# Performance work log

Hardware: AMD Instinct MI355X
Metric: run time of the kernel (lower is better)

## Reference

```python
import jax, jax.numpy as jnp
import numpy as np

DIM = 512
EPS = 1e-08
LN_EPS = 1e-05  # torch LayerNorm default


def layer_norm(x, g, b):
    mu = jnp.mean(x, axis=-1, keepdims=True)
    var = jnp.mean(jnp.square(x - mu), axis=-1, keepdims=True)
    return (x - mu) * jax.lax.rsqrt(var + LN_EPS) * g + b


def setup_inputs() -> dict:
    key = jax.random.key(0)
    ks = jax.random.split(key, 10)
    B, NQ, NK, D = 8, 1024, 2048, DIM
    s = 1.0 / np.sqrt(D)
    return {
        "inputs": jax.random.normal(ks[0], (B, NQ, D), jnp.float32),
        "context": jax.random.normal(ks[1], (B, NK, D), jnp.float32),
        "ln_in_g": jnp.ones((D,), jnp.float32),
        "ln_in_b": jnp.zeros((D,), jnp.float32),
        "ln_ctx_g": jnp.ones((D,), jnp.float32),
        "ln_ctx_b": jnp.zeros((D,), jnp.float32),
        "Wq": jax.random.uniform(ks[2], (D, D), jnp.float32, -s, s),
        "bq": jax.random.uniform(ks[3], (D,), jnp.float32, -s, s),
        "Wk": jax.random.uniform(ks[4], (D, D), jnp.float32, -s, s),
        "bk": jax.random.uniform(ks[5], (D,), jnp.float32, -s, s),
        "Wv": jax.random.uniform(ks[6], (D, D), jnp.float32, -s, s),
        "bv": jax.random.uniform(ks[7], (D,), jnp.float32, -s, s),
    }


def reference(inputs, context, ln_in_g, ln_in_b, ln_ctx_g, ln_ctx_b, Wq, bq, Wk, bk, Wv, bv):
    x = layer_norm(inputs, ln_in_g, ln_in_b)
    c = layer_norm(context, ln_ctx_g, ln_ctx_b)
    q = x @ Wq.T + bq  # [B, Nq, D]
    k = c @ Wk.T + bk  # [B, Nk, D]
    v = c @ Wv.T + bv  # [B, Nk, D]
    scale = DIM ** (-0.5)
    dots = jnp.einsum('bid,bjd->bij', q, k) * scale  # [B, Nq, Nk]
    attn = jax.nn.softmax(dots, axis=1) + EPS  # softmax over query axis
    attn = attn / jnp.sum(attn, axis=2, keepdims=True)  # renorm over key axis
    updates = jnp.einsum('bjd,bij->bid', v, attn)
    return updates
```

## Files before the change

kernel.cpp:

```cpp
#include <hip/hip_runtime.h>

using u16 = unsigned short;
typedef __attribute__((ext_vector_type(8))) short short8;
typedef __attribute__((ext_vector_type(4))) float floatx4;

#define NQ 1024
#define NK 2048
#define DD 512

__device__ __forceinline__ float bf2f(u16 u) {
  union { unsigned u; float f; } x; x.u = ((unsigned)u) << 16; return x.f;
}
__device__ __forceinline__ unsigned cvt_pk_bf16(float lo, float hi) {
  unsigned r;
  asm("v_cvt_pk_bf16_f32 %0, %1, %2" : "=v"(r) : "v"(lo), "v"(hi));
  return r;
}
__device__ __forceinline__ float wave_sum(float v) {
#pragma unroll
  for (int off = 32; off > 0; off >>= 1) v += __shfl_down(v, off, 64);
  return v;
}
__device__ __forceinline__ void gload16(const u16* g, const u16* l) {
  __builtin_amdgcn_global_load_lds(
      (const __attribute__((address_space(1))) void*)g,
      (__attribute__((address_space(3))) void*)l, 16, 0, 0);
}

__global__ __launch_bounds__(256) void ln_prep(
    const float* __restrict__ X1, const float* __restrict__ G1,
    const float* __restrict__ B1, u16* __restrict__ Y1,
    const float* __restrict__ X2, const float* __restrict__ G2,
    const float* __restrict__ B2, u16* __restrict__ Y2,
    const float* __restrict__ Wq, const float* __restrict__ Wk,
    const float* __restrict__ Wv, u16* __restrict__ wqb,
    u16* __restrict__ wkb, u16* __restrict__ wvb, float* __restrict__ Zero,
    float qsc) {
  const int bx = blockIdx.x;
  const int t = threadIdx.x;
  if (bx >= 6144) {
    int e = bx - 6144;
    if (e < 768) {
      const float* src = e < 256 ? Wq : (e < 512 ? Wk : Wv);
      u16* dst = e < 256 ? wqb : (e < 512 ? wkb : wvb);
      const float ws = e < 256 ? qsc : 1.f;
      int i = ((e & 255) * 256 + t) * 4;
      float4 v = *(const float4*)(src + i);
      union { unsigned u[2]; ushort4 s; } ou;
      ou.u[0] = cvt_pk_bf16(v.x * ws, v.y * ws);
      ou.u[1] = cvt_pk_bf16(v.z * ws, v.w * ws);
      *(ushort4*)(dst + i) = ou.s;
    } else {
      int i = ((e - 768) * 256 + t) * 4;
      float4 z = {0.f, 0.f, 0.f, 0.f};
      *(float4*)(Zero + i) = z;
    }
    return;
  }
  const int wave = t >> 6, lane = t & 63;
  int row = bx * 4 + wave;
  const float *X, *G, *Bv; u16* Y;
  if (row < 8192) { X = X1; G = G1; Bv = B1; Y = Y1; }
  else { row -= 8192; X = X2; G = G2; Bv = B2; Y = Y2; }
  const float4* Xp = (const float4*)(X + (long)row * DD);
  float4 v0 = Xp[lane * 2], v1 = Xp[lane * 2 + 1];
  float s = v0.x + v0.y + v0.z + v0.w + v1.x + v1.y + v1.z + v1.w;
  float ss = v0.x * v0.x + v0.y * v0.y + v0.z * v0.z + v0.w * v0.w +
             v1.x * v1.x + v1.y * v1.y + v1.z * v1.z + v1.w * v1.w;
  s = wave_sum(s);  s = __shfl(s, 0, 64);
  ss = wave_sum(ss); ss = __shfl(ss, 0, 64);
  float mu = s * (1.f / DD);
  float var = ss * (1.f / DD) - mu * mu;
  float rs = rsqrtf(var + 1e-5f);
  const float4* Gp = (const float4*)G;
  const float4* Bp = (const float4*)Bv;
  float4 g0 = Gp[lane * 2], g1 = Gp[lane * 2 + 1];
  float4 b0 = Bp[lane * 2], b1 = Bp[lane * 2 + 1];
  union { unsigned u[4]; short8 s8; } ou;
  ou.u[0] = cvt_pk_bf16((v0.x - mu) * rs * g0.x + b0.x,
                        (v0.y - mu) * rs * g0.y + b0.y);
  ou.u[1] = cvt_pk_bf16((v0.z - mu) * rs * g0.z + b0.z,
                        (v0.w - mu) * rs * g0.w + b0.w);
  ou.u[2] = cvt_pk_bf16((v1.x - mu) * rs * g1.x + b1.x,
                        (v1.y - mu) * rs * g1.y + b1.y);
  ou.u[3] = cvt_pk_bf16((v1.z - mu) * rs * g1.z + b1.z,
                        (v1.w - mu) * rs * g1.w + b1.w);
  *(short8*)(Y + (long)row * DD + lane * 8) = ou.s8;
}

__global__ __launch_bounds__(256) void gemm_proj(
    const u16* __restrict__ A1, const u16* __restrict__ W1,
    const float* __restrict__ b1, u16* __restrict__ C1,
    const u16* __restrict__ A2, const u16* __restrict__ W2,
    const float* __restrict__ b2, u16* __restrict__ C2,
    float bsc1, float bsc2) {
  __shared__ u16 smem[16384];
  u16* lA = smem;
  u16* lB = smem + 8192;
  const u16 *A, *B; const float* bias; u16* Cout; float bsc;
  int m0 = blockIdx.x * 128;
  if (blockIdx.x < 64) { A = A1; B = W1; bias = b1; Cout = C1; bsc = bsc1; }
  else { A = A2; B = W2; bias = b2; Cout = C2; bsc = bsc2;
         m0 = (blockIdx.x - 64) * 128; }
  const int n0 = blockIdx.y * 128;
  const int t = threadIdx.x, wave = t >> 6, lane = t & 63;
  const int fm = lane & 15, fq = lane >> 4;
  const int wm = (wave >> 1) * 64, wn = (wave & 1) * 64;

  const int srow = t >> 3;
  const int swz = ((t & 7) ^ (srow & 7)) * 8;
  const u16* gA = A + (long)(m0 + srow) * 512 + swz;
  const u16* gB = B + (long)(n0 + srow) * 512 + swz;
  u16* dA = lA + wave * 512;
  u16* dB = lB + wave * 512;

  floatx4 acc[4][4];
#pragma unroll
  for (int x = 0; x < 4; ++x)
#pragma unroll
    for (int y = 0; y < 4; ++y) { floatx4 z = {0.f, 0.f, 0.f, 0.f}; acc[x][y] = z; }

#pragma unroll 1
  for (int kt = 0; kt < 8; ++kt) {
    gload16(gA, dA);
    gload16(gA + 32L * 512, dA + 2048);
    gload16(gA + 64L * 512, dA + 4096);
    gload16(gA + 96L * 512, dA + 6144);
    gload16(gB, dB);
    gload16(gB + 32L * 512, dB + 2048);
    gload16(gB + 64L * 512, dB + 4096);
    gload16(gB + 96L * 512, dB + 6144);
    gA += 64; gB += 64;
    __syncthreads();
#pragma unroll
    for (int ks = 0; ks < 2; ++ks) {
      short8 af[4], bfr[4];
      const int csl = ((ks * 4 + fq) ^ (fm & 7)) * 8;
#pragma unroll
      for (int x = 0; x < 4; ++x)
        af[x] = *(const short8*)&lA[(wm + x * 16 + fm) * 64 + csl];
#pragma unroll
      for (int y = 0; y < 4; ++y)
        bfr[y] = *(const short8*)&lB[(wn + y * 16 + fm) * 64 + csl];
#pragma unroll
      for (int x = 0; x < 4; ++x)
#pragma unroll
        for (int y = 0; y < 4; ++y)
          acc[x][y] = __builtin_amdgcn_mfma_f32_16x16x32_bf16(af[x], bfr[y], acc[x][y], 0, 0, 0);
    }
    __syncthreads();
  }

  float bs[4];
  int cs[4];
#pragma unroll
  for (int y = 0; y < 4; ++y) {
    bs[y] = bias[n0 + wn + y * 16 + fm] * bsc;
    cs[y] = ((((wn >> 4) + y) ^ fq) * 16) + fm;
  }
#pragma unroll
  for (int x = 0; x < 4; ++x)
#pragma unroll
    for (int r = 0; r < 4; ++r) {
      int rowl = wm + x * 16 + fq * 4 + r;
      unsigned p01 = cvt_pk_bf16(acc[x][0][r] + bs[0], acc[x][1][r] + bs[1]);
      unsigned p23 = cvt_pk_bf16(acc[x][2][r] + bs[2], acc[x][3][r] + bs[3]);
      smem[rowl * 128 + cs[0]] = (u16)p01;
      smem[rowl * 128 + cs[1]] = (u16)(p01 >> 16);
      smem[rowl * 128 + cs[2]] = (u16)p23;
      smem[rowl * 128 + cs[3]] = (u16)(p23 >> 16);
    }
  __syncthreads();
#pragma unroll
  for (int p = 0; p < 8; ++p) {
    int rowl = p * 16 + (t >> 4);
    int c = t & 15;
    int q = (rowl >> 2) & 3;
    short8 v = *(const short8*)&smem[rowl * 128 + (((c >> 1) ^ q) * 16) + (c & 1) * 8];
    *(short8*)(Cout + (long)(m0 + rowl) * 512 + n0 + c * 8) = v;
  }
}

__global__ __launch_bounds__(256) void qk_vproj(
    const u16* __restrict__ qb, const u16* __restrict__ kb,
    u16* __restrict__ E, float* __restrict__ Z,
    const u16* __restrict__ wvb, const u16* __restrict__ cb,
    const float* __restrict__ bv, u16* __restrict__ vT,
    float* __restrict__ colV) {
  __shared__ u16 smem[16384];
  u16* lA = smem;
  u16* lB = smem + 8192;

  const int bx = blockIdx.x;
  const bool is_qk = bx < 1024;
  const u16 *A, *B;
  int m0, n0, b;
  if (is_qk) {
    b = bx & 7;
    n0 = ((bx >> 3) & 15) * 128;
    m0 = (bx >> 7) * 128;
    A = qb + (long)b * (1024L * 512);
    B = kb + (long)b * (2048L * 512);
  } else {
    int e = bx - 1024;
    m0 = (e & 3) * 128;
    n0 = (e >> 2) * 128;
    b = 0;
    A = wvb;
    B = cb;
  }
  const int t = threadIdx.x, wave = t >> 6, lane = t & 63;
  const int fm = lane & 15, fq = lane >> 4;
  const int wm = (wave >> 1) * 64, wn = (wave & 1) * 64;

  const int srow = t >> 3;
  const int swz = ((t & 7) ^ (srow & 7)) * 8;
  const u16* gA = A + (long)(m0 + srow) * 512 + swz;
  const u16* gB = B + (long)(n0 + srow) * 512 + swz;
  u16* dA = lA + wave * 512;
  u16* dB = lB + wave * 512;

  floatx4 acc[4][4];
#pragma unroll
  for (int x = 0; x < 4; ++x)
#pragma unroll
    for (int y = 0; y < 4; ++y) { floatx4 z = {0.f, 0.f, 0.f, 0.f}; acc[x][y] = z; }

#pragma unroll 1
  for (int kt = 0; kt < 8; ++kt) {
    gload16(gA, dA);
    gload16(gA + 32L * 512, dA + 2048);
    gload16(gA + 64L * 512, dA + 4096);
    gload16(gA + 96L * 512, dA + 6144);
    gload16(gB, dB);
    gload16(gB + 32L * 512, dB + 2048);
    gload16(gB + 64L * 512, dB + 4096);
    gload16(gB + 96L * 512, dB + 6144);
    gA += 64; gB += 64;
    __syncthreads();
#pragma unroll
    for (int ks = 0; ks < 2; ++ks) {
      short8 af[4], bfr[4];
      const int csl = ((ks * 4 + fq) ^ (fm & 7)) * 8;
#pragma unroll
      for (int x = 0; x < 4; ++x)
        af[x] = *(const short8*)&lA[(wm + x * 16 + fm) * 64 + csl];
#pragma unroll
      for (int y = 0; y < 4; ++y)
        bfr[y] = *(const short8*)&lB[(wn + y * 16 + fm) * 64 + csl];
#pragma unroll
      for (int x = 0; x < 4; ++x)
#pragma unroll
        for (int y = 0; y < 4; ++y)
          acc[x][y] = __builtin_amdgcn_mfma_f32_16x16x32_bf16(af[x], bfr[y], acc[x][y], 0, 0, 0);
    }
    __syncthreads();
  }

  int cs[4];
#pragma unroll
  for (int y = 0; y < 4; ++y) cs[y] = ((((wn >> 4) + y) ^ fq) * 16) + fm;

  if (is_qk) {
    float s4[4] = {0.f, 0.f, 0.f, 0.f};
#pragma unroll
    for (int x = 0; x < 4; ++x)
#pragma unroll
      for (int r = 0; r < 4; ++r) {
        int rowl = wm + x * 16 + fq * 4 + r;
        float e0 = __builtin_amdgcn_exp2f(acc[x][0][r]);
        float e1 = __builtin_amdgcn_exp2f(acc[x][1][r]);
        float e2 = __builtin_amdgcn_exp2f(acc[x][2][r]);
        float e3 = __builtin_amdgcn_exp2f(acc[x][3][r]);
        s4[0] += e0; s4[1] += e1; s4[2] += e2; s4[3] += e3;
        unsigned p01 = cvt_pk_bf16(e0, e1);
        unsigned p23 = cvt_pk_bf16(e2, e3);
        smem[rowl * 128 + cs[0]] = (u16)p01;
        smem[rowl * 128 + cs[1]] = (u16)(p01 >> 16);
        smem[rowl * 128 + cs[2]] = (u16)p23;
        smem[rowl * 128 + cs[3]] = (u16)(p23 >> 16);
      }
#pragma unroll
    for (int y = 0; y < 4; ++y) {
      s4[y] += __shfl_xor(s4[y], 16, 64);
      s4[y] += __shfl_xor(s4[y], 32, 64);
    }
    __syncthreads();
    u16* Eg = E + (long)b * (1024L * 2048);
#pragma unroll
    for (int p = 0; p < 8; ++p) {
      int rowl = p * 16 + (t >> 4);
      int c = t & 15;
      int q = (rowl >> 2) & 3;
      short8 v = *(const short8*)&smem[rowl * 128 + (((c >> 1) ^ q) * 16) + (c & 1) * 8];
      *(short8*)(Eg + (long)(m0 + rowl) * 2048 + n0 + c * 8) = v;
    }
    if (fq == 0) {
#pragma unroll
      for (int y = 0; y < 4; ++y)
        atomicAdd(&Z[b * 2048 + n0 + wn + y * 16 + fm], s4[y]);
    }
  } else {
    const int bb = n0 >> 11;
    const int j0c = n0 & 2047;
    float bsr[4][4];
#pragma unroll
    for (int x = 0; x < 4; ++x)
#pragma unroll
      for (int r = 0; r < 4; ++r)
        bsr[x][r] = bv[m0 + wm + x * 16 + fq * 4 + r];
    float rs[4][4];
#pragma unroll
    for (int x = 0; x < 4; ++x)
#pragma unroll
      for (int r = 0; r < 4; ++r) rs[x][r] = 0.f;
#pragma unroll
    for (int x = 0; x < 4; ++x)
#pragma unroll
      for (int r = 0; r < 4; ++r) {
        int rowl = wm + x * 16 + fq * 4 + r;
        float v0 = acc[x][0][r] + bsr[x][r];
        float v1 = acc[x][1][r] + bsr[x][r];
        float v2 = acc[x][2][r] + bsr[x][r];
        float v3 = acc[x][3][r] + bsr[x][r];
        rs[x][r] += v0 + v1 + v2 + v3;
        unsigned p01 = cvt_pk_bf16(v0, v1);
        unsigned p23 = cvt_pk_bf16(v2, v3);
        smem[rowl * 128 + cs[0]] = (u16)p01;
        smem[rowl * 128 + cs[1]] = (u16)(p01 >> 16);
        smem[rowl * 128 + cs[2]] = (u16)p23;
        smem[rowl * 128 + cs[3]] = (u16)(p23 >> 16);
      }
    __syncthreads();
    u16* Cg = vT + (long)bb * (512L * 2048) + j0c;
#pragma unroll
    for (int p = 0; p < 8; ++p) {
      int rowl = p * 16 + (t >> 4);
      int c = t & 15;
      int q = (rowl >> 2) & 3;
      short8 v = *(const short8*)&smem[rowl * 128 + (((c >> 1) ^ q) * 16) + (c & 1) * 8];
      *(short8*)(Cg + (long)(m0 + rowl) * 2048 + c * 8) = v;
    }
#pragma unroll
    for (int x = 0; x < 4; ++x)
#pragma unroll
      for (int r = 0; r < 4; ++r) {
        float s = rs[x][r];
        s += __shfl_xor(s, 1, 64);
        s += __shfl_xor(s, 2, 64);
        s += __shfl_xor(s, 4, 64);
        s += __shfl_xor(s, 8, 64);
        if (fm == 0)
          atomicAdd(&colV[bb * 512 + m0 + wm + x * 16 + fq * 4 + r], s);
      }
  }
}

__global__ __launch_bounds__(256) void gemm_pv(const u16* __restrict__ E,
    const u16* __restrict__ V, const float* __restrict__ colV,
    const float* __restrict__ Z, float* __restrict__ out) {
  __shared__ u16 smem[8192];
  __shared__ u16 sZb[2048];
  u16* lA = smem;
  u16* lB = smem + 4096;
  const int id = blockIdx.x;
  const int b = id & 7;
  const int m0 = ((id >> 3) & 15) * 64, n0 = (id >> 7) * 64;
  const int t = threadIdx.x, wave = t >> 6, lane = t & 63;
  const int fm = lane & 15, fq = lane >> 4;
  const int wm = (wave >> 1) * 32, wn = (wave & 1) * 32;

  {
    int i = t * 8;
    float4 z0 = *(const float4*)(Z + b * 2048 + i);
    float4 z1 = *(const float4*)(Z + b * 2048 + i + 4);
    union { unsigned u[4]; short8 s8; } o;
    o.u[0] = cvt_pk_bf16(__builtin_amdgcn_rcpf(z0.x), __builtin_amdgcn_rcpf(z0.y));
    o.u[1] = cvt_pk_bf16(__builtin_amdgcn_rcpf(z0.z), __builtin_amdgcn_rcpf(z0.w));
    o.u[2] = cvt_pk_bf16(__builtin_amdgcn_rcpf(z1.x), __builtin_amdgcn_rcpf(z1.y));
    o.u[3] = cvt_pk_bf16(__builtin_amdgcn_rcpf(z1.z), __builtin_amdgcn_rcpf(z1.w));
    *(short8*)&sZb[i] = o.s8;
  }
  __syncthreads();

  const int srow = t >> 3;
  const int swz = ((t & 7) ^ (srow & 7)) * 8;
  const u16* gA = E + (long)b * (1024L * 2048) + (long)(m0 + srow) * 2048 + swz;
  const u16* gB = V + (long)b * (512L * 2048) + (long)(n0 + srow) * 2048 + swz;
  u16* dA = lA + wave * 512;
  u16* dB = lB + wave * 512;

  floatx4 acc[2][2];
  floatx4 accR[2];
#pragma unroll
  for (int x = 0; x < 2; ++x) {
    floatx4 z = {0.f, 0.f, 0.f, 0.f};
    accR[x] = z;
#pragma unroll
    for (int y = 0; y < 2; ++y) acc[x][y] = z;
  }

  short8 rv0 = *(const short8*)gB;
  short8 rv1 = *(const short8*)(gB + 32L * 2048);
  gB += 64;

#pragma unroll 1
  for (int kt = 0; kt < 32; ++kt) {
    gload16(gA, dA);
    gload16(gA + 32L * 2048, dA + 2048);
    gA += 64;
    short8 zr = *(const short8*)&sZb[kt * 64 + swz];
    union { unsigned u[4]; short8 s8; } o0, o1;
#pragma unroll
    for (int e = 0; e < 4; ++e) {
      float zlo = bf2f((u16)zr[2 * e]), zhi = bf2f((u16)zr[2 * e + 1]);
      o0.u[e] = cvt_pk_bf16(bf2f((u16)rv0[2 * e]) * zlo,
                            bf2f((u16)rv0[2 * e + 1]) * zhi);
      o1.u[e] = cvt_pk_bf16(bf2f((u16)rv1[2 * e]) * zlo,
                            bf2f((u16)rv1[2 * e + 1]) * zhi);
    }
    u16* db = dB + (lane << 3);
    *(short8*)db = o0.s8;
    *(short8*)(db + 2048) = o1.s8;
    if (kt < 31) {
      rv0 = *(const short8*)gB;
      rv1 = *(const short8*)(gB + 32L * 2048);
      gB += 64;
    }
    __syncthreads();
#pragma unroll
    for (int ks = 0; ks < 2; ++ks) {
      short8 af[2], bfr[2];
      const int chunk = ks * 4 + fq;
      const int csl = (chunk ^ (fm & 7)) * 8;
#pragma unroll
      for (int x = 0; x < 2; ++x)
        af[x] = *(const short8*)&lA[(wm + x * 16 + fm) * 64 + csl];
#pragma unroll
      for (int y = 0; y < 2; ++y)
        bfr[y] = *(const short8*)&lB[(wn + y * 16 + fm) * 64 + csl];
      short8 zf = *(const short8*)&sZb[kt * 64 + chunk * 8];
#pragma unroll
      for (int x = 0; x < 2; ++x) {
#pragma unroll
        for (int y = 0; y < 2; ++y)
          acc[x][y] = __builtin_amdgcn_mfma_f32_16x16x32_bf16(af[x], bfr[y], acc[x][y], 0, 0, 0);
        accR[x] = __builtin_amdgcn_mfma_f32_16x16x32_bf16(af[x], zf, accR[x], 0, 0, 0);
      }
    }
    __syncthreads();
  }

  float cv[2];
#pragma unroll
  for (int y = 0; y < 2; ++y) cv[y] = colV[b * 512 + n0 + wn + y * 16 + fm];
  float* sO = (float*)smem;
#pragma unroll
  for (int x = 0; x < 2; ++x)
#pragma unroll
    for (int r = 0; r < 4; ++r) {
      float invR = __builtin_amdgcn_rcpf(accR[x][r] + 2048.f * 1e-8f);
      int rowl = wm + x * 16 + fq * 4 + r;
#pragma unroll
      for (int y = 0; y < 2; ++y) {
        const int cblk = (wn >> 4) + y;
        sO[rowl * 64 + ((cblk ^ fq) * 16) + fm] =
            (acc[x][y][r] + 1e-8f * cv[y]) * invR;
      }
    }
  __syncthreads();
  float* og = out + (long)b * (1024L * 512);
#pragma unroll
  for (int p = 0; p < 4; ++p) {
    int rowl = p * 16 + (t >> 4);
    int c = t & 15;
    int q = (rowl >> 2) & 3;
    float4 v = *(const float4*)&sO[rowl * 64 + (((c >> 2) ^ q) * 16) + (c & 3) * 4];
    *(float4*)(og + (long)(m0 + rowl) * 512 + n0 + c * 4) = v;
  }
}

extern "C" void kernel_launch(void* const* d_in, const int* in_sizes, int n_in,
                              void* d_out, int out_size, void* d_ws, size_t ws_size,
                              hipStream_t stream) {
  const float* inputs  = (const float*)d_in[0];
  const float* context = (const float*)d_in[1];
  const float* ln_in_g = (const float*)d_in[2];
  const float* ln_in_b = (const float*)d_in[3];
  const float* ln_ctx_g = (const float*)d_in[4];
  const float* ln_ctx_b = (const float*)d_in[5];
  const float* Wq = (const float*)d_in[6];
  const float* bq = (const float*)d_in[7];
  const float* Wk = (const float*)d_in[8];
  const float* bk = (const float*)d_in[9];
  const float* Wv = (const float*)d_in[10];
  const float* bv = (const float*)d_in[11];
  float* out = (float*)d_out;

  u16* ws = (u16*)d_ws;
  u16* xb  = ws;
  u16* qb  = xb + 8192L * 512;
  u16* cb  = qb + 8192L * 512;
  u16* wqb = cb + 16384L * 512;
  u16* wkb = wqb + 512L * 512;
  u16* wvb = wkb + 512L * 512;
  u16* kb  = wvb + 512L * 512;
  u16* vTs = kb + 16384L * 512;
  u16* E   = vTs + 8L * 512 * 2048;
  float* Z    = (float*)(E + 8L * 1024 * 2048);
  float* colV = Z + 8L * 2048;

  const float qsc = (float)(0.04419417382415922 * 1.4426950408889634);

  ln_prep<<<6932, 256, 0, stream>>>(inputs, ln_in_g, ln_in_b, xb,
                                    context, ln_ctx_g, ln_ctx_b, cb,
                                    Wq, Wk, Wv, wqb, wkb, wvb, Z, qsc);
  gemm_proj<<<dim3(192, 4, 1), 256, 0, stream>>>(xb, wqb, bq, qb,
                                                 cb, wkb, bk, kb, qsc, 1.f);
  qk_vproj<<<1536, 256, 0, stream>>>(qb, kb, E, Z, wvb, cb, bv, vTs, colV);
  gemm_pv<<<1024, 256, 0, stream>>>(E, vTs, colV, Z, out);
}
```

Before: 209.3 us.

## Fuse K and V projections sharing context tiles; separate QK GEMM kernel

```diff
diff --git a/kernel.cpp b/kernel.cpp
--- a/kernel.cpp
+++ b/kernel.cpp
@@ -88,21 +88,226 @@
   *(short8*)(Y + (long)row * DD + lane * 8) = ou.s8;
 }
 
-__global__ __launch_bounds__(256) void gemm_proj(
-    const u16* __restrict__ A1, const u16* __restrict__ W1,
-    const float* __restrict__ b1, u16* __restrict__ C1,
-    const u16* __restrict__ A2, const u16* __restrict__ W2,
-    const float* __restrict__ b2, u16* __restrict__ C2,
-    float bsc1, float bsc2) {
+__global__ __launch_bounds__(256) void proj_all(
+    const u16* __restrict__ xb, const u16* __restrict__ wqb,
+    const float* __restrict__ bq, u16* __restrict__ qb,
+    const u16* __restrict__ cb, const u16* __restrict__ wkb,
+    const float* __restrict__ bk, u16* __restrict__ kb,
+    const u16* __restrict__ wvb, const float* __restrict__ bv,
+    u16* __restrict__ vT, float* __restrict__ colV, float qsc) {
+  __shared__ u16 smem[16384];
+  const int bx = blockIdx.x;
+  const int t = threadIdx.x, wave = t >> 6, lane = t & 63;
+  const int fm = lane & 15, fq = lane >> 4;
+  const int srow = t >> 3;
+  const int swz = ((t & 7) ^ (srow & 7)) * 8;
+
+  if (bx < 256) {
+    u16* lA = smem;
+    u16* lB = smem + 8192;
+    const int m0 = (bx >> 2) * 128, n0 = (bx & 3) * 128;
+    const int wm = (wave >> 1) * 64, wn = (wave & 1) * 64;
+    const u16* gA = xb + (long)(m0 + srow) * 512 + swz;
+    const u16* gB = wqb + (long)(n0 + srow) * 512 + swz;
+    u16* dA = lA + wave * 512;
+    u16* dB = lB + wave * 512;
+
+    floatx4 acc[4][4];
+#pragma unroll
+    for (int x = 0; x < 4; ++x)
+#pragma unroll
+      for (int y = 0; y < 4; ++y) { floatx4 z = {0.f,0.f,0.f,0.f}; acc[x][y] = z; }
+
+#pragma unroll 1
+    for (int kt = 0; kt < 8; ++kt) {
+      gload16(gA, dA);
+      gload16(gA + 32L * 512, dA + 2048);
+      gload16(gA + 64L * 512, dA + 4096);
+      gload16(gA + 96L * 512, dA + 6144);
+      gload16(gB, dB);
+      gload16(gB + 32L * 512, dB + 2048);
+      gload16(gB + 64L * 512, dB + 4096);
+      gload16(gB + 96L * 512, dB + 6144);
+      gA += 64; gB += 64;
+      __syncthreads();
+#pragma unroll
+      for (int ks = 0; ks < 2; ++ks) {
+        short8 af[4], bfr[4];
+        const int csl = ((ks * 4 + fq) ^ (fm & 7)) * 8;
+#pragma unroll
+        for (int x = 0; x < 4; ++x)
+          af[x] = *(const short8*)&lA[(wm + x * 16 + fm) * 64 + csl];
+#pragma unroll
+        for (int y = 0; y < 4; ++y)
+          bfr[y] = *(const short8*)&lB[(wn + y * 16 + fm) * 64 + csl];
+#pragma unroll
+        for (int x = 0; x < 4; ++x)
+#pragma unroll
+          for (int y = 0; y < 4; ++y)
+            acc[x][y] = __builtin_amdgcn_mfma_f32_16x16x32_bf16(af[x], bfr[y], acc[x][y], 0, 0, 0);
+      }
+      __syncthreads();
+    }
+
+    float bs[4];
+    int cs[4];
+#pragma unroll
+    for (int y = 0; y < 4; ++y) {
+      bs[y] = bq[n0 + wn + y * 16 + fm] * qsc;
+      cs[y] = ((((wn >> 4) + y) ^ fq) * 16) + fm;
+    }
+#pragma unroll
+    for (int x = 0; x < 4; ++x)
+#pragma unroll
+      for (int r = 0; r < 4; ++r) {
+        int rowl = wm + x * 16 + fq * 4 + r;
+        unsigned p01 = cvt_pk_bf16(acc[x][0][r] + bs[0], acc[x][1][r] + bs[1]);
+        unsigned p23 = cvt_pk_bf16(acc[x][2][r] + bs[2], acc[x][3][r] + bs[3]);
+        smem[rowl * 128 + cs[0]] = (u16)p01;
+        smem[rowl * 128 + cs[1]] = (u16)(p01 >> 16);
+        smem[rowl * 128 + cs[2]] = (u16)p23;
+        smem[rowl * 128 + cs[3]] = (u16)(p23 >> 16);
+      }
+    __syncthreads();
+#pragma unroll
+    for (int p = 0; p < 8; ++p) {
+      int rowl = p * 16 + (t >> 4);
+      int c = t & 15;
+      int q = (rowl >> 2) & 3;
+      short8 v = *(const short8*)&smem[rowl * 128 + (((c >> 1) ^ q) * 16) + (c & 1) * 8];
+      *(short8*)(qb + (long)(m0 + rowl) * 512 + n0 + c * 8) = v;
+    }
+  } else {
+    const int e = bx - 256;
+    const int j0 = (e >> 3) * 128, d0 = (e & 7) * 64;
+    const int bb = j0 >> 11, j0c = j0 & 2047;
+    u16* lA = smem;
+    u16* lK = smem + 8192;
+    u16* lV = smem + 12288;
+    const int wm = (wave >> 1) * 64, wn = (wave & 1) * 32;
+    const u16* gA = cb + (long)(j0 + srow) * 512 + swz;
+    const u16* gK = wkb + (long)(d0 + srow) * 512 + swz;
+    const u16* gV = wvb + (long)(d0 + srow) * 512 + swz;
+    u16* dA = lA + wave * 512;
+    u16* dK = lK + wave * 512;
+    u16* dV = lV + wave * 512;
+
+    floatx4 aK[4][2], aV[4][2];
+#pragma unroll
+    for (int x = 0; x < 4; ++x)
+#pragma unroll
+      for (int y = 0; y < 2; ++y) {
+        floatx4 z = {0.f, 0.f, 0.f, 0.f};
+        aK[x][y] = z; aV[x][y] = z;
+      }
+
+#pragma unroll 1
+    for (int kt = 0; kt < 8; ++kt) {
+      gload16(gA, dA);
+      gload16(gA + 32L * 512, dA + 2048);
+      gload16(gA + 64L * 512, dA + 4096);
+      gload16(gA + 96L * 512, dA + 6144);
+      gload16(gK, dK);
+      gload16(gK + 32L * 512, dK + 2048);
+      gload16(gV, dV);
+      gload16(gV + 32L * 512, dV + 2048);
+      gA += 64; gK += 64; gV += 64;
+      __syncthreads();
+#pragma unroll
+      for (int ks = 0; ks < 2; ++ks) {
+        short8 af[4], bk8[2], bv8[2];
+        const int csl = ((ks * 4 + fq) ^ (fm & 7)) * 8;
+#pragma unroll
+        for (int x = 0; x < 4; ++x)
+          af[x] = *(const short8*)&lA[(wm + x * 16 + fm) * 64 + csl];
+#pragma unroll
+        for (int y = 0; y < 2; ++y) {
+          bk8[y] = *(const short8*)&lK[(wn + y * 16 + fm) * 64 + csl];
+          bv8[y] = *(const short8*)&lV[(wn + y * 16 + fm) * 64 + csl];
+        }
+#pragma unroll
+        for (int x = 0; x < 4; ++x)
+#pragma unroll
+          for (int y = 0; y < 2; ++y) {
+            aK[x][y] = __builtin_amdgcn_mfma_f32_16x16x32_bf16(af[x], bk8[y], aK[x][y], 0, 0, 0);
+            aV[x][y] = __builtin_amdgcn_mfma_f32_16x16x32_bf16(af[x], bv8[y], aV[x][y], 0, 0, 0);
+          }
+      }
+      __syncthreads();
+    }
+
+    u16* sK = smem;
+    u16* sV = smem + 8192;
+    float bks[2], bvs[2];
+    int dloc[2];
+#pragma unroll
+    for (int y = 0; y < 2; ++y) {
+      dloc[y] = wn + y * 16 + fm;
+      bks[y] = bk[d0 + dloc[y]];
+      bvs[y] = bv[d0 + dloc[y]];
+    }
+    float cva[2] = {0.f, 0.f};
+#pragma unroll
+    for (int x = 0; x < 4; ++x)
+#pragma unroll
+      for (int r = 0; r < 4; ++r) {
+        int rowl = wm + x * 16 + fq * 4 + r;
+        float vk0 = aK[x][0][r] + bks[0];
+        float vk1 = aK[x][1][r] + bks[1];
+        float vv0 = aV[x][0][r] + bvs[0];
+        float vv1 = aV[x][1][r] + bvs[1];
+        cva[0] += vv0; cva[1] += vv1;
+        unsigned pk = cvt_pk_bf16(vk0, vk1);
+        unsigned pv = cvt_pk_bf16(vv0, vv1);
+        const int ck0 = ((((wn >> 4) + 0) ^ fq) * 16) + fm;
+        const int ck1 = ((((wn >> 4) + 1) ^ fq) * 16) + fm;
+        sK[rowl * 64 + ck0] = (u16)pk;
+        sK[rowl * 64 + ck1] = (u16)(pk >> 16);
+        const int jblk = rowl >> 4, jin = rowl & 15;
+        sV[dloc[0] * 128 + ((jblk ^ (dloc[0] & 7)) * 16) + jin] = (u16)pv;
+        sV[dloc[1] * 128 + ((jblk ^ (dloc[1] & 7)) * 16) + jin] = (u16)(pv >> 16);
+      }
+    __syncthreads();
+#pragma unroll
+    for (int p = 0; p < 4; ++p) {
+      int rowl = p * 32 + (t >> 3);
+      int c = t & 7;
+      int q = (rowl >> 2) & 3;
+      short8 v = *(const short8*)&sK[rowl * 64 + (((c >> 1) ^ q) * 16) + (c & 1) * 8];
+      *(short8*)(kb + (long)(j0 + rowl) * 512 + d0 + c * 8) = v;
+    }
+    u16* Vg = vT + (long)bb * (512L * 2048) + j0c;
+#pragma unroll
+    for (int p = 0; p < 4; ++p) {
+      int d = p * 16 + (t >> 4);
+      int c = t & 15;
+      short8 v = *(const short8*)&sV[d * 128 + (((c >> 1) ^ (d & 7)) * 16) + (c & 1) * 8];
+      *(short8*)(Vg + (long)(d0 + d) * 2048 + c * 8) = v;
+    }
+#pragma unroll
+    for (int y = 0; y < 2; ++y) {
+      float s = cva[y];
+      s += __shfl_xor(s, 16, 64);
+      s += __shfl_xor(s, 32, 64);
+      if (fq == 0) atomicAdd(&colV[bb * 512 + d0 + dloc[y]], s);
+    }
+  }
+}
+
+__global__ __launch_bounds__(256) void gemm_qk(
+    const u16* __restrict__ qb, const u16* __restrict__ kb,
+    u16* __restrict__ E, float* __restrict__ Z) {
   __shared__ u16 smem[16384];
   u16* lA = smem;
   u16* lB = smem + 8192;
-  const u16 *A, *B; const float* bias; u16* Cout; float bsc;
-  int m0 = blockIdx.x * 128;
-  if (blockIdx.x < 64) { A = A1; B = W1; bias = b1; Cout = C1; bsc = bsc1; }
-  else { A = A2; B = W2; bias = b2; Cout = C2; bsc = bsc2;
-         m0 = (blockIdx.x - 64) * 128; }
-  const int n0 = blockIdx.y * 128;
+
+  const int bx = blockIdx.x;
+  const int b = bx & 7;
+  const int n0 = ((bx >> 3) & 15) * 128;
+  const int m0 = (bx >> 7) * 128;
+  const u16* A = qb + (long)b * (1024L * 512);
+  const u16* B = kb + (long)b * (2048L * 512);
+
   const int t = threadIdx.x, wave = t >> 6, lane = t & 63;
   const int fm = lane & 15, fq = lane >> 4;
   const int wm = (wave >> 1) * 64, wn = (wave & 1) * 64;
@@ -151,208 +356,47 @@
     __syncthreads();
   }
 
-  float bs[4];
   int cs[4];
 #pragma unroll
-  for (int y = 0; y < 4; ++y) {
-    bs[y] = bias[n0 + wn + y * 16 + fm] * bsc;
-    cs[y] = ((((wn >> 4) + y) ^ fq) * 16) + fm;
-  }
+  for (int y = 0; y < 4; ++y) cs[y] = ((((wn >> 4) + y) ^ fq) * 16) + fm;
+
+  float s4[4] = {0.f, 0.f, 0.f, 0.f};
 #pragma unroll
   for (int x = 0; x < 4; ++x)
 #pragma unroll
     for (int r = 0; r < 4; ++r) {
       int rowl = wm + x * 16 + fq * 4 + r;
-      unsigned p01 = cvt_pk_bf16(acc[x][0][r] + bs[0], acc[x][1][r] + bs[1]);
-      unsigned p23 = cvt_pk_bf16(acc[x][2][r] + bs[2], acc[x][3][r] + bs[3]);
+      float e0 = __builtin_amdgcn_exp2f(acc[x][0][r]);
+      float e1 = __builtin_amdgcn_exp2f(acc[x][1][r]);
+      float e2 = __builtin_amdgcn_exp2f(acc[x][2][r]);
+      float e3 = __builtin_amdgcn_exp2f(acc[x][3][r]);
+      s4[0] += e0; s4[1] += e1; s4[2] += e2; s4[3] += e3;
+      unsigned p01 = cvt_pk_bf16(e0, e1);
+      unsigned p23 = cvt_pk_bf16(e2, e3);
       smem[rowl * 128 + cs[0]] = (u16)p01;
       smem[rowl * 128 + cs[1]] = (u16)(p01 >> 16);
       smem[rowl * 128 + cs[2]] = (u16)p23;
       smem[rowl * 128 + cs[3]] = (u16)(p23 >> 16);
     }
+#pragma unroll
+  for (int y = 0; y < 4; ++y) {
+    s4[y] += __shfl_xor(s4[y], 16, 64);
+    s4[y] += __shfl_xor(s4[y], 32, 64);
+  }
   __syncthreads();
+  u16* Eg = E + (long)b * (1024L * 2048);
 #pragma unroll
   for (int p = 0; p < 8; ++p) {
     int rowl = p * 16 + (t >> 4);
     int c = t & 15;
     int q = (rowl >> 2) & 3;
     short8 v = *(const short8*)&smem[rowl * 128 + (((c >> 1) ^ q) * 16) + (c & 1) * 8];
-    *(short8*)(Cout + (long)(m0 + rowl) * 512 + n0 + c * 8) = v;
-  }
-}
-
-__global__ __launch_bounds__(256) void qk_vproj(
-    const u16* __restrict__ qb, const u16* __restrict__ kb,
-    u16* __restrict__ E, float* __restrict__ Z,
-    const u16* __restrict__ wvb, const u16* __restrict__ cb,
-    const float* __restrict__ bv, u16* __restrict__ vT,
-    float* __restrict__ colV) {
-  __shared__ u16 smem[16384];
-  u16* lA = smem;
-  u16* lB = smem + 8192;
-
-  const int bx = blockIdx.x;
-  const bool is_qk = bx < 1024;
-  const u16 *A, *B;
-  int m0, n0, b;
-  if (is_qk) {
-    b = bx & 7;
-    n0 = ((bx >> 3) & 15) * 128;
-    m0 = (bx >> 7) * 128;
-    A = qb + (long)b * (1024L * 512);
-    B = kb + (long)b * (2048L * 512);
-  } else {
-    int e = bx - 1024;
-    m0 = (e & 3) * 128;
-    n0 = (e >> 2) * 128;
-    b = 0;
-    A = wvb;
-    B = cb;
-  }
-  const int t = threadIdx.x, wave = t >> 6, lane = t & 63;
-  const int fm = lane & 15, fq = lane >> 4;
-  const int wm = (wave >> 1) * 64, wn = (wave & 1) * 64;
-
-  const int srow = t >> 3;
-  const int swz = ((t & 7) ^ (srow & 7)) * 8;
-  const u16* gA = A + (long)(m0 + srow) * 512 + swz;
-  const u16* gB = B + (long)(n0 + srow) * 512 + swz;
-  u16* dA = lA + wave * 512;
-  u16* dB = lB + wave * 512;
-
-  floatx4 acc[4][4];
-#pragma unroll
-  for (int x = 0; x < 4; ++x)
-#pragma unroll
-    for (int y = 0; y < 4; ++y) { floatx4 z = {0.f, 0.f, 0.f, 0.f}; acc[x][y] = z; }
-
-#pragma unroll 1
-  for (int kt = 0; kt < 8; ++kt) {
-    gload16(gA, dA);
-    gload16(gA + 32L * 512, dA + 2048);
-    gload16(gA + 64L * 512, dA + 4096);
-    gload16(gA + 96L * 512, dA + 6144);
-    gload16(gB, dB);
-    gload16(gB + 32L * 512, dB + 2048);
-    gload16(gB + 64L * 512, dB + 4096);
-    gload16(gB + 96L * 512, dB + 6144);
-    gA += 64; gB += 64;
-    __syncthreads();
-#pragma unroll
-    for (int ks = 0; ks < 2; ++ks) {
-      short8 af[4], bfr[4];
-      const int csl = ((ks * 4 + fq) ^ (fm & 7)) * 8;
-#pragma unroll
-      for (int x = 0; x < 4; ++x)
-        af[x] = *(const short8*)&lA[(wm + x * 16 + fm) * 64 + csl];
-#pragma unroll
-      for (int y = 0; y < 4; ++y)
-        bfr[y] = *(const short8*)&lB[(wn + y * 16 + fm) * 64 + csl];
-#pragma unroll
-      for (int x = 0; x < 4; ++x)
-#pragma unroll
-        for (int y = 0; y < 4; ++y)
-          acc[x][y] = __builtin_amdgcn_mfma_f32_16x16x32_bf16(af[x], bfr[y], acc[x][y], 0, 0, 0);
-    }
-    __syncthreads();
-  }
-
-  int cs[4];
-#pragma unroll
-  for (int y = 0; y < 4; ++y) cs[y] = ((((wn >> 4) + y) ^ fq) * 16) + fm;
-
-  if (is_qk) {
-    float s4[4] = {0.f, 0.f, 0.f, 0.f};
-#pragma unroll
-    for (int x = 0; x < 4; ++x)
-#pragma unroll
-      for (int r = 0; r < 4; ++r) {
-        int rowl = wm + x * 16 + fq * 4 + r;
-        float e0 = __builtin_amdgcn_exp2f(acc[x][0][r]);
-        float e1 = __builtin_amdgcn_exp2f(acc[x][1][r]);
-        float e2 = __builtin_amdgcn_exp2f(acc[x][2][r]);
-        float e3 = __builtin_amdgcn_exp2f(acc[x][3][r]);
-        s4[0] += e0; s4[1] += e1; s4[2] += e2; s4[3] += e3;
-        unsigned p01 = cvt_pk_bf16(e0, e1);
-        unsigned p23 = cvt_pk_bf16(e2, e3);
-        smem[rowl * 128 + cs[0]] = (u16)p01;
-        smem[rowl * 128 + cs[1]] = (u16)(p01 >> 16);
-        smem[rowl * 128 + cs[2]] = (u16)p23;
-        smem[rowl * 128 + cs[3]] = (u16)(p23 >> 16);
-      }
-#pragma unroll
-    for (int y = 0; y < 4; ++y) {
-      s4[y] += __shfl_xor(s4[y], 16, 64);
-      s4[y] += __shfl_xor(s4[y], 32, 64);
-    }
-    __syncthreads();
-    u16* Eg = E + (long)b * (1024L * 2048);
-#pragma unroll
-    for (int p = 0; p < 8; ++p) {
-      int rowl = p * 16 + (t >> 4);
-      int c = t & 15;
-      int q = (rowl >> 2) & 3;
-      short8 v = *(const short8*)&smem[rowl * 128 + (((c >> 1) ^ q) * 16) + (c & 1) * 8];
-      *(short8*)(Eg + (long)(m0 + rowl) * 2048 + n0 + c * 8) = v;
-    }
-    if (fq == 0) {
-#pragma unroll
-      for (int y = 0; y < 4; ++y)
-        atomicAdd(&Z[b * 2048 + n0 + wn + y * 16 + fm], s4[y]);
-    }
-  } else {
-    const int bb = n0 >> 11;
-    const int j0c = n0 & 2047;
-    float bsr[4][4];
-#pragma unroll
-    for (int x = 0; x < 4; ++x)
-#pragma unroll
-      for (int r = 0; r < 4; ++r)
-        bsr[x][r] = bv[m0 + wm + x * 16 + fq * 4 + r];
-    float rs[4][4];
-#pragma unroll
-    for (int x = 0; x < 4; ++x)
-#pragma unroll
-      for (int r = 0; r < 4; ++r) rs[x][r] = 0.f;
-#pragma unroll
-    for (int x = 0; x < 4; ++x)
-#pragma unroll
-      for (int r = 0; r < 4; ++r) {
-        int rowl = wm + x * 16 + fq * 4 + r;
-        float v0 = acc[x][0][r] + bsr[x][r];
-        float v1 = acc[x][1][r] + bsr[x][r];
-        float v2 = acc[x][2][r] + bsr[x][r];
-        float v3 = acc[x][3][r] + bsr[x][r];
-        rs[x][r] += v0 + v1 + v2 + v3;
-        unsigned p01 = cvt_pk_bf16(v0, v1);
-        unsigned p23 = cvt_pk_bf16(v2, v3);
-        smem[rowl * 128 + cs[0]] = (u16)p01;
-        smem[rowl * 128 + cs[1]] = (u16)(p01 >> 16);
-        smem[rowl * 128 + cs[2]] = (u16)p23;
-        smem[rowl * 128 + cs[3]] = (u16)(p23 >> 16);
-      }
-    __syncthreads();
-    u16* Cg = vT + (long)bb * (512L * 2048) + j0c;
-#pragma unroll
-    for (int p = 0; p < 8; ++p) {
-      int rowl = p * 16 + (t >> 4);
-      int c = t & 15;
-      int q = (rowl >> 2) & 3;
-      short8 v = *(const short8*)&smem[rowl * 128 + (((c >> 1) ^ q) * 16) + (c & 1) * 8];
-      *(short8*)(Cg + (long)(m0 + rowl) * 2048 + c * 8) = v;
-    }
-#pragma unroll
-    for (int x = 0; x < 4; ++x)
-#pragma unroll
-      for (int r = 0; r < 4; ++r) {
-        float s = rs[x][r];
-        s += __shfl_xor(s, 1, 64);
-        s += __shfl_xor(s, 2, 64);
-        s += __shfl_xor(s, 4, 64);
-        s += __shfl_xor(s, 8, 64);
-        if (fm == 0)
-          atomicAdd(&colV[bb * 512 + m0 + wm + x * 16 + fq * 4 + r], s);
-      }
+    *(short8*)(Eg + (long)(m0 + rowl) * 2048 + n0 + c * 8) = v;
+  }
+  if (fq == 0) {
+#pragma unroll
+    for (int y = 0; y < 4; ++y)
+      atomicAdd(&Z[b * 2048 + n0 + wn + y * 16 + fm], s4[y]);
   }
 }
 
@@ -515,8 +559,9 @@
   ln_prep<<<6932, 256, 0, stream>>>(inputs, ln_in_g, ln_in_b, xb,
                                     context, ln_ctx_g, ln_ctx_b, cb,
                                     Wq, Wk, Wv, wqb, wkb, wvb, Z, qsc);
-  gemm_proj<<<dim3(192, 4, 1), 256, 0, stream>>>(xb, wqb, bq, qb,
-                                                 cb, wkb, bk, kb, qsc, 1.f);
-  qk_vproj<<<1536, 256, 0, stream>>>(qb, kb, E, Z, wvb, cb, bv, vTs, colV);
+  proj_all<<<1280, 256, 0, stream>>>(xb, wqb, bq, qb,
+                                     cb, wkb, bk, kb,
+                                     wvb, bv, vTs, colV, qsc);
+  gemm_qk<<<1024, 256, 0, stream>>>(qb, kb, E, Z);
   gemm_pv<<<1024, 256, 0, stream>>>(E, vTs, colV, Z, out);
 }
```

Result: no change. 212.8 us (+1.7%).
